# Performance work log

Hardware: AMD Instinct MI355X
Metric: run time of the kernel (lower is better)

Reference implementation:

```python
import jax, jax.numpy as jnp
import numpy as np

B, N, D, H = 4, 2048, 256, 4
DH = D // H          # 64
SCALE = DH ** (-0.5)
LN_EPS = 1e-5


def setup_inputs() -> dict:
    key = jax.random.key(0)
    ks = jax.random.split(key, 16)
    g = lambda k, shape, fan_in: jax.random.normal(k, shape, jnp.float32) / np.sqrt(fan_in)
    # Weights stored as [in, out] (pre-transposed vs torch Linear)
    return {
        "x0": jax.random.normal(ks[0], (B, N, D), jnp.float32),
        "x1": jax.random.normal(ks[1], (B, N, D), jnp.float32),
        "Wqk": g(ks[2], (D, D), D), "bqk": jnp.zeros((D,), jnp.float32),
        "Wv": g(ks[3], (D, D), D), "bv": jnp.zeros((D,), jnp.float32),
        "Wout": g(ks[4], (D, D), D), "bout": jnp.zeros((D,), jnp.float32),
        "Wf1": g(ks[5], (2 * D, 2 * D), 2 * D), "bf1": jnp.zeros((2 * D,), jnp.float32),
        "ln_g": jnp.ones((2 * D,), jnp.float32), "ln_b": jnp.zeros((2 * D,), jnp.float32),
        "Wf2": g(ks[6], (2 * D, D), 2 * D), "bf2": jnp.zeros((D,), jnp.float32),
    }


def _split_heads(t):
    # [B,N,D] -> [B,H,N,DH]
    b, n, _ = t.shape
    return t.reshape(b, n, H, DH).transpose(0, 2, 1, 3)


def _merge_heads(t):
    # [B,H,N,DH] -> [B,N,D]
    b, h, n, dh = t.shape
    return t.transpose(0, 2, 1, 3).reshape(b, n, h * dh)


def _layernorm(x, g, b):
    mu = jnp.mean(x, axis=-1, keepdims=True)
    var = jnp.mean(jnp.square(x - mu), axis=-1, keepdims=True)
    return (x - mu) * jax.lax.rsqrt(var + LN_EPS) * g + b


def reference(x0, x1, Wqk, bqk, Wv, bv, Wout, bout, Wf1, bf1, ln_g, ln_b, Wf2, bf2):
    qk0 = _split_heads(x0 @ Wqk + bqk)   # [B,H,N,DH]
    qk1 = _split_heads(x1 @ Wqk + bqk)
    v0 = _split_heads(x0 @ Wv + bv)
    v1 = _split_heads(x1 @ Wv + bv)

    ss = SCALE ** 0.5
    sim = jnp.einsum('bhid,bhjd->bhij', qk0 * ss, qk1 * ss)  # shared score matrix
    attn01 = jax.nn.softmax(sim, axis=-1)   # normalize over j
    attn10 = jax.nn.softmax(sim, axis=-2)   # normalize over i (== softmax(sim^T) transposed)
    m0 = jnp.einsum('bhij,bhjd->bhid', attn01, v1)
    m1 = jnp.einsum('bhji,bhjd->bhid', attn10, v0)

    m0 = _merge_heads(m0) @ Wout + bout   # [B,N,D]
    m1 = _merge_heads(m1) @ Wout + bout

    def ffn(x):
        h = x @ Wf1 + bf1                 # [B,N,2D]
        h = jax.nn.gelu(_layernorm(h, ln_g, ln_b), approximate=False)
        return h @ Wf2 + bf2              # [B,N,D]

    y0 = x0 + ffn(jnp.concatenate([x0, m0], axis=-1))
    y1 = x1 + ffn(jnp.concatenate([x1, m1], axis=-1))
    return (y0, y1)
```

## Files before the change

kernel.cpp:

```cpp
#include <hip/hip_runtime.h>
#include <hip/hip_bf16.h>
#include <math.h>

typedef __bf16 bf16;
typedef __attribute__((ext_vector_type(8))) __bf16 bf16x8;
typedef __attribute__((ext_vector_type(4))) __bf16 bf16x4;
typedef __attribute__((ext_vector_type(2))) __bf16 bf16x2;
typedef __attribute__((ext_vector_type(4))) float f32x4;
typedef __attribute__((ext_vector_type(16))) float f32x16;
typedef __attribute__((ext_vector_type(4))) unsigned u32x4;

#define MFMA(a,b,c)   __builtin_amdgcn_mfma_f32_16x16x32_bf16(a,b,c,0,0,0)
#define MFMA32(a,b,c) __builtin_amdgcn_mfma_f32_32x32x16_bf16(a,b,c,0,0,0)

static constexpr int Bb = 4, Nn = 2048, Hh = 4;
static constexpr float SS2 = 0.4246609001440095f;

__device__ __forceinline__ void lds16(const bf16* src, bf16* dst) {
  __builtin_amdgcn_global_load_lds(
      (const __attribute__((address_space(1))) void*)src,
      (__attribute__((address_space(3))) void*)dst, 16, 0, 0);
}

__device__ __forceinline__ f32x16 zero16() {
  f32x16 t;
#pragma unroll
  for (int i = 0; i < 16; ++i) t[i] = 0.f;
  return t;
}

__global__ __launch_bounds__(256) void prep_k(
    const float* Wqk, const float* Wv, const float* Wout, const float* bout,
    const float* Wf1, const float* Wf2, const float* x0, const float* x1,
    bf16* wqkv_t, bf16* wout_b, bf16* wfold_t, bf16* wf1b_t, bf16* wf2_t,
    bf16* xb0, bf16* xb1) {
  const int bid = blockIdx.x, tid = threadIdx.x;
  if (bid < 128) {
    __shared__ float LT[64][65];
    const float* src; bf16* dst;
    int srcLD, dstLD, r0, c0, rbase;
    int t = bid;
    if (t < 16) {
      src = Wqk; srcLD = 256; r0 = (t >> 2) * 64; c0 = (t & 3) * 64;
      dst = wqkv_t; dstLD = 256; rbase = 0;
    } else if (t < 32) { t -= 16;
      src = Wv; srcLD = 256; r0 = (t >> 2) * 64; c0 = (t & 3) * 64;
      dst = wqkv_t + 256 * 256; dstLD = 256; rbase = 0;
    } else if (t < 64) { t -= 32;
      src = Wf1; srcLD = 512; r0 = (t >> 3) * 64; c0 = (t & 7) * 64;
      dst = wfold_t; dstLD = 512; rbase = 0;
    } else if (t < 96) { t -= 64;
      src = Wf1; srcLD = 512; r0 = 256 + (t >> 3) * 64; c0 = (t & 7) * 64;
      dst = wf1b_t; dstLD = 256; rbase = 256;
    } else { t -= 96;
      src = Wf2; srcLD = 256; r0 = (t >> 2) * 64; c0 = (t & 3) * 64;
      dst = wf2_t; dstLD = 512; rbase = 0;
    }
#pragma unroll
    for (int i = 0; i < 4; ++i) {
      int rr = (tid >> 4) + i * 16;
      int cc = (tid & 15) * 4;
      f32x4 v = *reinterpret_cast<const f32x4*>(&src[(size_t)(r0 + rr) * srcLD + c0 + cc]);
      LT[rr][cc] = v[0]; LT[rr][cc + 1] = v[1]; LT[rr][cc + 2] = v[2]; LT[rr][cc + 3] = v[3];
    }
    __syncthreads();
    int n = tid >> 2, kc = (tid & 3) * 16;
    bf16x8 o0, o1;
#pragma unroll
    for (int i = 0; i < 8; ++i) o0[i] = (bf16)LT[kc + i][n];
#pragma unroll
    for (int i = 0; i < 8; ++i) o1[i] = (bf16)LT[kc + 8 + i][n];
    bf16* dp = dst + (size_t)(c0 + n) * dstLD + (r0 - rbase) + kc;
    *reinterpret_cast<bf16x8*>(dp) = o0;
    *reinterpret_cast<bf16x8*>(dp + 8) = o1;
    return;
  }
  int id = bid - 128;
  if (id < 96) {
    int base = id * 1024 + tid * 4;
#pragma unroll
    for (int i = 0; i < 4; ++i) {
      int e = base + i;
      if (e < 65536) wout_b[e] = (bf16)Wout[e];
      else { int id3 = e - 65536; int r = id3 >> 8, k = id3 & 255;
             wout_b[e] = (r == 0) ? (bf16)bout[k] : (bf16)0.f; }
    }
    return;
  }
  id -= 96;
  if (id < 4096) {
    int j = id * 256 + tid;
    const float* xs = (j < 524288) ? x0 : x1;
    bf16* xd = (j < 524288) ? xb0 : xb1;
    int jj = (j < 524288) ? j : j - 524288;
    f32x4 v = *reinterpret_cast<const f32x4*>(&xs[(size_t)jj * 4]);
    bf16x4 o; o[0] = (bf16)v[0]; o[1] = (bf16)v[1]; o[2] = (bf16)v[2]; o[3] = (bf16)v[3];
    *reinterpret_cast<bf16x4*>(&xd[(size_t)jj * 4]) = o;
  }
}

__global__ __launch_bounds__(256, 2) void qkvfold_k(
    const bf16* xb0, const bf16* xb1, const bf16* wqkv_t,
    const float* bqk, const float* bv,
    bf16* qks0, bf16* qks1, bf16* vT0, bf16* vT1,
    const bf16* wout_b, const bf16* wf1b_t, const float* bf1,
    bf16* wfold_t, float* bfold) {
  const int fid = blockIdx.x;
  const bool fold = fid >= 512;
  int bx, by, bz;
  if (!fold) {
    bx = ((fid & 7) << 3) + ((fid >> 3) & 7);
    by = (fid >> 6) & 3;
    bz = fid >> 8;
  } else {
    int id = fid - 512;
    bx = id % 3; by = id / 3; bz = 0;
  }

  const bf16* Aa = fold ? wout_b : (bz ? xb1 : xb0);
  const bf16* Wt = fold ? wf1b_t : wqkv_t;

  const int tid = threadIdx.x;
  const int lane = tid & 63;
  const int w = tid >> 6;
  const int wr = w >> 1, wc = w & 1;
  const int m0r = bx * 128;
  const int n0 = by * 128;
  const int r15 = lane & 15, g = lane >> 4, rb = r15 & 7;
  const int l3 = lane >> 3, l7 = lane & 7;
  const int swzc = (l7 ^ l3) * 8;

  __shared__ bf16 At[2][8192];
  __shared__ bf16 Bt[2][8192];

  const bf16* aA = Aa + (size_t)(m0r + w*32 + l3) * 256 + swzc;
  const bf16* bB = Wt + (size_t)(n0 + w*32 + l3) * 256 + swzc;
  const int adst = (w*32) * 64;

  auto stage = [&](int buf, int kc) {
#pragma unroll
    for (int i = 0; i < 4; i++)
      lds16(aA + kc*64 + (size_t)i * 8 * 256, &At[buf][adst + i*512]);
#pragma unroll
    for (int i = 0; i < 4; i++)
      lds16(bB + kc*64 + (size_t)i * 8 * 256, &Bt[buf][adst + i*512]);
  };

  f32x4 acc[4][4];
#pragma unroll
  for (int i = 0; i < 4; i++)
#pragma unroll
    for (int j = 0; j < 4; j++) acc[i][j] = f32x4{0.f, 0.f, 0.f, 0.f};

  const int rx0 = ((0*4 + g) ^ rb) << 4;
  const int rx1 = ((1*4 + g) ^ rb) << 4;

  auto compute = [&](int cur) {
    const char* Ap = (const char*)&At[cur][0];
    const char* Bp = (const char*)&Bt[cur][0];
    __builtin_amdgcn_s_setprio(1);
#pragma unroll
    for (int ks = 0; ks < 2; ++ks) {
      const int rx = ks ? rx1 : rx0;
      bf16x8 af[4], bfr[4];
#pragma unroll
      for (int mf = 0; mf < 4; ++mf)
        af[mf] = *reinterpret_cast<const bf16x8*>(Ap + (wr*64 + mf*16 + r15) * 128 + rx);
#pragma unroll
      for (int nf = 0; nf < 4; ++nf)
        bfr[nf] = *reinterpret_cast<const bf16x8*>(Bp + (wc*64 + nf*16 + r15) * 128 + rx);
#pragma unroll
      for (int mf = 0; mf < 4; ++mf)
#pragma unroll
        for (int nf = 0; nf < 4; ++nf)
          acc[mf][nf] = MFMA(af[mf], bfr[nf], acc[mf][nf]);
    }
    __builtin_amdgcn_s_setprio(0);
  };

  stage(0, 0);
  int cur = 0;
  for (int kc = 0; kc < 3; ++kc) {
    stage(cur ^ 1, kc + 1);
    asm volatile("s_waitcnt vmcnt(8)" ::: "memory");
    __builtin_amdgcn_sched_barrier(0);
    __builtin_amdgcn_s_barrier();
    __builtin_amdgcn_sched_barrier(0);
    compute(cur);
    asm volatile("s_waitcnt lgkmcnt(0)" ::: "memory");
    __builtin_amdgcn_sched_barrier(0);
    __builtin_amdgcn_s_barrier();
    __builtin_amdgcn_sched_barrier(0);
    cur ^= 1;
  }
  asm volatile("s_waitcnt vmcnt(0)" ::: "memory");
  __builtin_amdgcn_sched_barrier(0);
  __builtin_amdgcn_s_barrier();
  __builtin_amdgcn_sched_barrier(0);
  compute(cur);

  if (!fold) {
    bf16* qks = bz ? qks1 : qks0;
    bf16* vT  = bz ? vT1  : vT0;
    if (by < 2) {
#pragma unroll
      for (int mf = 0; mf < 4; ++mf)
#pragma unroll
        for (int nf = 0; nf < 4; ++nf) {
          f32x4 c = acc[mf][nf];
          int cg = n0 + wc*64 + nf*16 + r15;
#pragma unroll
          for (int r = 0; r < 4; ++r) {
            int rg = m0r + wr*64 + mf*16 + g*4 + r;
            int b = rg >> 11, n = rg & 2047;
            float val = (c[r] + bqk[cg]) * SS2;
            int h = cg >> 6, dh = cg & 63;
            qks[(((size_t)(b*Hh + h)) * Nn + n) * 64 + dh] = (bf16)val;
          }
        }
    } else {
      __syncthreads();
      char* T = (char*)&At[0][0];
#pragma unroll
      for (int mf = 0; mf < 4; ++mf)
#pragma unroll
        for (int nf = 0; nf < 4; ++nf) {
          f32x4 c = acc[mf][nf];
          int cl = wc*64 + nf*16 + r15;
          float bvv = bv[(by - 2) * 128 + cl];
          int rl = wr*64 + mf*16 + g*4;
          bf16x4 o;
          o[0] = (bf16)(c[0] + bvv); o[1] = (bf16)(c[1] + bvv);
          o[2] = (bf16)(c[2] + bvv); o[3] = (bf16)(c[3] + bvv);
          int boff = cl*256 + ((rl*2) ^ ((cl & 15) << 4));
          *reinterpret_cast<bf16x4*>(T + boff) = o;
        }
      __syncthreads();
      const int cl = tid >> 1, nh = tid & 1;
      const int c2 = (by - 2) * 128 + cl;
      const int h = c2 >> 6, dh = c2 & 63;
      const int b = m0r >> 11, nbase = (m0r & 2047) + nh*64;
      bf16* dst = vT + (((size_t)(b*Hh + h)) * 64 + dh) * 2048 + nbase;
#pragma unroll
      for (int i = 0; i < 8; ++i) {
        int nl = nh*64 + i*8;
        int boff = cl*256 + ((nl*2) ^ ((cl & 15) << 4));
        *reinterpret_cast<uint4*>(dst + i*8) = *reinterpret_cast<const uint4*>(T + boff);
      }
    }
  } else {
#pragma unroll
    for (int mf = 0; mf < 4; ++mf)
#pragma unroll
      for (int nf = 0; nf < 4; ++nf) {
        f32x4 c = acc[mf][nf];
        int cg = n0 + wc*64 + nf*16 + r15;
#pragma unroll
        for (int r = 0; r < 4; ++r) {
          int rg = m0r + wr*64 + mf*16 + g*4 + r;
          if (rg < 256) wfold_t[(size_t)cg * 512 + 256 + rg] = (bf16)c[r];
          else if (rg == 256) bfold[cg] = c[r] + bf1[cg];
        }
      }
  }
}

template<int MODE, int BN, int MINW, int REMAP>
__global__ __launch_bounds__(256, MINW) void gemm_k(
    const bf16* Aa0, const bf16* Aa1, const bf16* Ac0, const bf16* Ac1,
    const bf16* Wt, const float* bias,
    bf16* ob0, bf16* ob1, float* of0, float* of1) {
  constexpr int KD  = 512;
  constexpr int LDA = (MODE == 4) ? 512 : 256;
  constexpr int NKC = KD / 64;
  constexpr int NF  = BN / 32;

  int bx = blockIdx.x, by = blockIdx.y, bz = blockIdx.z;
  if constexpr (REMAP == 1) {
    int id = blockIdx.x + 64 * (blockIdx.y + 4 * blockIdx.z);
    bx = ((id & 7) << 3) + ((id >> 3) & 7);
    by = (id >> 6) & 3;
    bz = id >> 8;
  }

  const bf16* Aa = bz ? Aa1 : Aa0;
  const bf16* Ac = bz ? Ac1 : Ac0;
  bf16*  ob = bz ? ob1 : ob0;
  float* of = bz ? of1 : of0;

  const int tid = threadIdx.x;
  const int lane = tid & 63;
  const int w = tid >> 6;
  const int wr = w >> 1, wc = w & 1;
  const int m0r = bx * 128;
  const int n0 = by * BN;
  const int r15 = lane & 15, g = lane >> 4, rb = r15 & 7;
  const int l3 = lane >> 3, l7 = lane & 7;
  const int swzc = (l7 ^ l3) * 8;

  __shared__ bf16 At[2][8192];
  __shared__ bf16 Bt[2][BN * 64];

  const bf16* aA = Aa + (size_t)(m0r + w*32 + l3) * LDA + swzc;
  const bf16* aC = (MODE == 3) ? (Ac + (size_t)(m0r + w*32 + l3) * 256 + swzc) : nullptr;
  const bf16* bB = Wt + (size_t)(n0 + w*(BN/4) + l3) * KD + swzc;
  const int adst = (w*32) * 64;
  const int bdst = (w*(BN/4)) * 64;

  auto stage = [&](int buf, int kc) {
    const bf16* ab; int kcol;
    if constexpr (MODE == 3) {
      if (kc < 4) { ab = aA; kcol = kc * 64; } else { ab = aC; kcol = (kc - 4) * 64; }
    } else { ab = aA; kcol = kc * 64; }
#pragma unroll
    for (int i = 0; i < 4; i++)
      lds16(ab + kcol + (size_t)i * 8 * LDA, &At[buf][adst + i*512]);
#pragma unroll
    for (int i = 0; i < NF; i++)
      lds16(bB + kc*64 + (size_t)i * 8 * KD, &Bt[buf][bdst + i*512]);
  };

  f32x4 acc[4][NF];
#pragma unroll
  for (int i = 0; i < 4; i++)
#pragma unroll
    for (int j = 0; j < NF; j++) acc[i][j] = f32x4{0.f, 0.f, 0.f, 0.f};

  const int rx0 = ((0*4 + g) ^ rb) << 4;
  const int rx1 = ((1*4 + g) ^ rb) << 4;

  auto compute = [&](int cur) {
    const char* Ap = (const char*)&At[cur][0];
    const char* Bp = (const char*)&Bt[cur][0];
    __builtin_amdgcn_s_setprio(1);
#pragma unroll
    for (int ks = 0; ks < 2; ++ks) {
      const int rx = ks ? rx1 : rx0;
      bf16x8 af[4], bfr[NF];
#pragma unroll
      for (int mf = 0; mf < 4; ++mf)
        af[mf] = *reinterpret_cast<const bf16x8*>(Ap + (wr*64 + mf*16 + r15) * 128 + rx);
#pragma unroll
      for (int nf = 0; nf < NF; ++nf)
        bfr[nf] = *reinterpret_cast<const bf16x8*>(Bp + (wc*(BN/2) + nf*16 + r15) * 128 + rx);
#pragma unroll
      for (int mf = 0; mf < 4; ++mf)
#pragma unroll
        for (int nf = 0; nf < NF; ++nf)
          acc[mf][nf] = MFMA(af[mf], bfr[nf], acc[mf][nf]);
    }
    __builtin_amdgcn_s_setprio(0);
  };

  stage(0, 0);
  int cur = 0;
  for (int kc = 0; kc < NKC - 1; ++kc) {
    stage(cur ^ 1, kc + 1);
    if constexpr (NF == 4) asm volatile("s_waitcnt vmcnt(8)" ::: "memory");
    else                   asm volatile("s_waitcnt vmcnt(6)" ::: "memory");
    __builtin_amdgcn_sched_barrier(0);
    __builtin_amdgcn_s_barrier();
    __builtin_amdgcn_sched_barrier(0);
    compute(cur);
    asm volatile("s_waitcnt lgkmcnt(0)" ::: "memory");
    __builtin_amdgcn_sched_barrier(0);
    __builtin_amdgcn_s_barrier();
    __builtin_amdgcn_sched_barrier(0);
    cur ^= 1;
  }
  asm volatile("s_waitcnt vmcnt(0)" ::: "memory");
  __builtin_amdgcn_sched_barrier(0);
  __builtin_amdgcn_s_barrier();
  __builtin_amdgcn_sched_barrier(0);
  compute(cur);

#pragma unroll
  for (int mf = 0; mf < 4; ++mf)
#pragma unroll
    for (int nf = 0; nf < NF; ++nf) {
      f32x4 c = acc[mf][nf];
      int cg = n0 + wc*(BN/2) + nf*16 + r15;
#pragma unroll
      for (int r = 0; r < 4; ++r) {
        int rg = m0r + wr*64 + mf*16 + g*4 + r;
        if constexpr (MODE == 3) {
          ob[(size_t)rg * 512 + cg] = (bf16)(c[r] + bias[cg]);
        } else {
          of[(size_t)rg * 256 + cg] = c[r] + bias[cg] + (float)Ac[(size_t)rg * 256 + cg];
        }
      }
    }
}

__global__ __launch_bounds__(512, 4) void attn_k(
    const bf16* qks0, const bf16* qks1, const bf16* vT0, const bf16* vT1,
    bf16* m0o, bf16* m1o) {
  const int B = blockIdx.x + 16 * (blockIdx.y + 16 * blockIdx.z);
  const int xcd = B & 7, kk = B >> 3;
  const int group = 4 * xcd + (kk >> 4);
  const int it = kk & 15;
  const int bh = group & 15, dir = group >> 4;

  const bf16* Q  = (dir ? qks1 : qks0) + (size_t)bh * (Nn * 64);
  const bf16* Kp = (dir ? qks0 : qks1) + (size_t)bh * (Nn * 64);
  const bf16* Vp = (dir ? vT0  : vT1 ) + (size_t)bh * (64 * Nn);
  bf16* out = dir ? m1o : m0o;
  const int b = bh >> 2, h = bh & 3;

  const int tid = threadIdx.x, lane = tid & 63, w = tid >> 6;
  const int ig = w >> 1, hj = w & 1;
  const int l31 = lane & 31, hi = lane >> 5, xr = l31 & 7;
  const int iw = it * 128 + ig * 32;

  __shared__ char smem[65536];
  bf16* KV = (bf16*)smem;
  const int kbase = hj * 8192;
  const int vbase = 16384 + hj * 8192;

  bf16x8 qf[4];
#pragma unroll
  for (int kt = 0; kt < 4; ++kt)
    qf[kt] = *reinterpret_cast<const bf16x8*>(
        &Q[(size_t)(iw + l31) * 64 + kt*16 + hi*8]);

  f32x16 acc[2]; acc[0] = zero16(); acc[1] = zero16();
  float rsum = 0.f;

  const int l3 = lane >> 3, l7 = lane & 7;
  const int swz = ((l7 ^ l3) * 8);
  const bf16* ks0 = Kp + (size_t)(ig*16 +     l3) * 64 + swz;
  const bf16* ks1 = Kp + (size_t)(ig*16 + 8 + l3) * 64 + swz;
  const bf16* vs0 = Vp + (size_t)(ig*16 +     l3) * 2048 + swz;
  const bf16* vs1 = Vp + (size_t)(ig*16 + 8 + l3) * 2048 + swz;
  const int kd0 = (ig*16    ) * 64;
  const int kd1 = (ig*16 + 8) * 64;

  auto stage = [&](int buf, int j0) {
    lds16(ks0 + (size_t)j0 * 64, KV + kbase + buf*4096 + kd0);
    lds16(ks1 + (size_t)j0 * 64, KV + kbase + buf*4096 + kd1);
    lds16(vs0 + j0,              KV + vbase + buf*4096 + kd0);
    lds16(vs1 + j0,              KV + vbase + buf*4096 + kd1);
  };

  int kby[2][4], vby[2][4];
#pragma unroll
  for (int jm = 0; jm < 2; ++jm)
#pragma unroll
    for (int kt = 0; kt < 4; ++kt)
      kby[jm][kt] = (jm*32 + l31) * 128 + (((2*kt + hi) ^ xr) << 4);
#pragma unroll
  for (int nt = 0; nt < 2; ++nt)
#pragma unroll
    for (int gg = 0; gg < 4; ++gg)
      vby[nt][gg] = (nt*32 + l31) * 128 + (((2*gg + hi) ^ xr) << 4);

  auto compute_tile = [&](int cur) {
    const char* Kb = (const char*)(KV + kbase + cur*4096);
    const char* Vb = (const char*)(KV + vbase + cur*4096);
    f32x16 st[2];
    __builtin_amdgcn_s_setprio(1);
#pragma unroll
    for (int jm = 0; jm < 2; ++jm) {
      f32x16 t = zero16();
#pragma unroll
      for (int kt = 0; kt < 4; ++kt) {
        bf16x8 kf = *reinterpret_cast<const bf16x8*>(Kb + kby[jm][kt]);
        t = MFMA32(kf, qf[kt], t);
      }
      st[jm] = t;
    }
    __builtin_amdgcn_s_setprio(0);
    bf16x8 pa[4];
#pragma unroll
    for (int jm = 0; jm < 2; ++jm) {
      unsigned dw[8];
#pragma unroll
      for (int s = 0; s < 8; ++s) {
        float e0 = __builtin_amdgcn_exp2f(st[jm][2*s]);
        float e1 = __builtin_amdgcn_exp2f(st[jm][2*s + 1]);
        rsum += e0 + e1;
        asm("v_cvt_pk_bf16_f32 %0, %1, %2" : "=v"(dw[s]) : "v"(e0), "v"(e1));
      }
#pragma unroll
      for (int kt2 = 0; kt2 < 2; ++kt2) {
        unsigned a0 = dw[4*kt2 + 0], b0 = dw[4*kt2 + 2];
        unsigned a1 = dw[4*kt2 + 1], b1 = dw[4*kt2 + 3];
        asm volatile("v_permlane32_swap_b32 %0, %1" : "+v"(a0), "+v"(b0));
        asm volatile("v_permlane32_swap_b32 %0, %1" : "+v"(a1), "+v"(b1));
        u32x4 uu; uu[0] = a0; uu[1] = a1; uu[2] = b0; uu[3] = b1;
        pa[jm*2 + kt2] = __builtin_bit_cast(bf16x8, uu);
      }
    }
    __builtin_amdgcn_s_setprio(1);
#pragma unroll
    for (int gg = 0; gg < 4; ++gg) {
#pragma unroll
      for (int nt = 0; nt < 2; ++nt) {
        bf16x8 vf = *reinterpret_cast<const bf16x8*>(Vb + vby[nt][gg]);
        acc[nt] = MFMA32(pa[gg], vf, acc[nt]);
      }
    }
    __builtin_amdgcn_s_setprio(0);
  };

  const int jt0 = hj << 4;
  stage(0, jt0 << 6);
  int cur = 0;
  for (int t = 0; t < 15; ++t) {
    stage(cur ^ 1, (jt0 + t + 1) << 6);
    asm volatile("s_waitcnt vmcnt(4)" ::: "memory");
    __builtin_amdgcn_s_barrier();
    compute_tile(cur);
    asm volatile("s_waitcnt lgkmcnt(0)" ::: "memory");
    __builtin_amdgcn_s_barrier();
    cur ^= 1;
  }
  asm volatile("s_waitcnt vmcnt(0)" ::: "memory");
  __builtin_amdgcn_s_barrier();
  compute_tile(cur);

  rsum += __shfl_xor(rsum, 32);
  __syncthreads();
  float* Ex = (float*)smem;
  if (hj == 1) {
#pragma unroll
    for (int nt = 0; nt < 2; ++nt)
#pragma unroll
      for (int r = 0; r < 16; ++r)
        Ex[(ig*33 + nt*16 + r) * 64 + lane] = acc[nt][r];
    Ex[(ig*33 + 32) * 64 + lane] = rsum;
  }
  __syncthreads();
  if (hj == 0) {
    float tot = rsum + Ex[(ig*33 + 32) * 64 + lane];
    float* Rt2 = (float*)(smem + 49152);
    if (lane < 32) Rt2[ig*32 + l31] = tot;
    f32x4 rv[4];
#pragma unroll
    for (int q = 0; q < 4; ++q)
      rv[q] = *reinterpret_cast<const f32x4*>(&Rt2[ig*32 + 8*q + 4*hi]);
#pragma unroll
    for (int r = 0; r < 16; ++r) {
      float inv = 1.0f / rv[r >> 2][r & 3];
      int row = iw + (r & 3) + 8*(r >> 2) + 4*hi;
#pragma unroll
      for (int nt = 0; nt < 2; ++nt) {
        float o = acc[nt][r] + Ex[(ig*33 + nt*16 + r) * 64 + lane];
        int col = h*64 + nt*32 + l31;
        out[((size_t)b * Nn + row) * 256 + col] = (bf16)(o * inv);
      }
    }
  }
}

__global__ __launch_bounds__(256) void ln_gelu_k(
    bf16* hg, const float* g, const float* bb) {
  const int row = (blockIdx.x << 2) + (threadIdx.x >> 6);
  const int lane = threadIdx.x & 63;
  bf16* hr = hg + (size_t)row * 512 + lane * 8;
  bf16x8 v = *reinterpret_cast<const bf16x8*>(hr);
  float f[8];
  float s = 0.f, sq = 0.f;
#pragma unroll
  for (int i = 0; i < 8; ++i) { f[i] = (float)v[i]; s += f[i]; sq += f[i]*f[i]; }
#pragma unroll
  for (int m = 1; m < 64; m <<= 1) { s += __shfl_xor(s, m); sq += __shfl_xor(sq, m); }
  float mu = s * (1.f / 512.f);
  float var = sq * (1.f / 512.f) - mu * mu;
  float rsv = rsqrtf(var + 1e-5f);
  f32x4 g0 = *reinterpret_cast<const f32x4*>(&g[lane*8]);
  f32x4 g1 = *reinterpret_cast<const f32x4*>(&g[lane*8 + 4]);
  f32x4 b0 = *reinterpret_cast<const f32x4*>(&bb[lane*8]);
  f32x4 b1 = *reinterpret_cast<const f32x4*>(&bb[lane*8 + 4]);
  bf16x8 o;
#pragma unroll
  for (int i = 0; i < 8; ++i) {
    float gv = (i < 4) ? g0[i] : g1[i-4];
    float bv = (i < 4) ? b0[i] : b1[i-4];
    float xn = (f[i] - mu) * rsv * gv + bv;
    float ge = 0.5f * xn * (1.f + erff(xn * 0.70710678118f));
    o[i] = (bf16)ge;
  }
  *reinterpret_cast<bf16x8*>(hr) = o;
}

extern "C" void kernel_launch(void* const* d_in, const int* in_sizes, int n_in,
                              void* d_out, int out_size, void* d_ws, size_t ws_size,
                              hipStream_t stream) {
  (void)in_sizes; (void)n_in; (void)out_size; (void)ws_size;
  const float* x0   = (const float*)d_in[0];
  const float* x1   = (const float*)d_in[1];
  const float* Wqk  = (const float*)d_in[2];
  const float* bqk  = (const float*)d_in[3];
  const float* Wv   = (const float*)d_in[4];
  const float* bv   = (const float*)d_in[5];
  const float* Wout = (const float*)d_in[6];
  const float* bout = (const float*)d_in[7];
  const float* Wf1  = (const float*)d_in[8];
  const float* bf1  = (const float*)d_in[9];
  const float* ln_g = (const float*)d_in[10];
  const float* ln_b = (const float*)d_in[11];
  const float* Wf2  = (const float*)d_in[12];
  const float* bf2  = (const float*)d_in[13];
  float* y = (float*)d_out;

  bf16* p = (bf16*)d_ws;
  bf16* wqkv_t = p; p += 131072;
  bf16* wout_b = p; p += 98304;
  bf16* wfold_t = p; p += 262144;
  bf16* wf1b_t = p; p += 131072;
  bf16* wf2_t  = p; p += 131072;
  float* bfold = (float*)p; p += 1024;
  bf16* xb0  = p; p += 2097152;
  bf16* xb1  = p; p += 2097152;
  bf16* qks0 = p; p += 2097152;
  bf16* qks1 = p; p += 2097152;
  bf16* vT0  = p; p += 2097152;
  bf16* vT1  = p; p += 2097152;
  bf16* m0   = p; p += 2097152;
  bf16* m1   = p; p += 2097152;
  bf16* hg0  = p; p += 4194304;
  bf16* hg1  = p; p += 4194304;

  dim3 blk(256);
  prep_k<<<4320, blk, 0, stream>>>(Wqk, Wv, Wout, bout, Wf1, Wf2, x0, x1,
                                   wqkv_t, wout_b, wfold_t, wf1b_t, wf2_t, xb0, xb1);
  qkvfold_k<<<dim3(524), blk, 0, stream>>>(
      xb0, xb1, wqkv_t, bqk, bv, qks0, qks1, vT0, vT1,
      wout_b, wf1b_t, bf1, wfold_t, bfold);
  attn_k<<<dim3(16, 16, 2), dim3(512), 0, stream>>>(qks0, qks1, vT0, vT1, m0, m1);
  gemm_k<3,128,2,1><<<dim3(64, 4, 2), blk, 0, stream>>>(
      xb0, xb1, m0, m1, wfold_t, bfold,
      hg0, hg1, nullptr, nullptr);
  ln_gelu_k<<<dim3(4096), blk, 0, stream>>>(hg0, ln_g, ln_b);
  gemm_k<4,64,3,0><<<dim3(64, 4, 2), blk, 0, stream>>>(
      hg0, hg1, xb0, xb1, wf2_t, bf2,
      nullptr, nullptr, y, y + 2097152);
}
```

Before: 110.6 us.

## Fuse x fp32->bf16 conversion into QKV GEMM and attention tail blocks

The QKV projection now reads x0/x1 directly as fp32 through registers and converts to bf16 while writing into LDS, instead of relying on a separate conversion pass in prep_k. The bf16 copies of x still needed by the later FFN GEMMs are produced by 512 extra blocks appended to the attention launch, so prep_k shrinks to weight preparation only. The GEMM pipeline is restructured so the global loads for the next tile are issued before compute and the LDS writes happen after it. This trades a separate memory pass for doubled fp32 A-tile read traffic and register-staged loads in the GEMM, and it adds tail work to the attention grid.

```diff
diff --git a/kernel.cpp b/kernel.cpp
--- a/kernel.cpp
+++ b/kernel.cpp
@@ -31,9 +31,8 @@
 
 __global__ __launch_bounds__(256) void prep_k(
     const float* Wqk, const float* Wv, const float* Wout, const float* bout,
-    const float* Wf1, const float* Wf2, const float* x0, const float* x1,
-    bf16* wqkv_t, bf16* wout_b, bf16* wfold_t, bf16* wf1b_t, bf16* wf2_t,
-    bf16* xb0, bf16* xb1) {
+    const float* Wf1, const float* Wf2,
+    bf16* wqkv_t, bf16* wout_b, bf16* wfold_t, bf16* wf1b_t, bf16* wf2_t) {
   const int bid = blockIdx.x, tid = threadIdx.x;
   if (bid < 128) {
     __shared__ float LT[64][65];
@@ -85,22 +84,11 @@
       else { int id3 = e - 65536; int r = id3 >> 8, k = id3 & 255;
              wout_b[e] = (r == 0) ? (bf16)bout[k] : (bf16)0.f; }
     }
-    return;
-  }
-  id -= 96;
-  if (id < 4096) {
-    int j = id * 256 + tid;
-    const float* xs = (j < 524288) ? x0 : x1;
-    bf16* xd = (j < 524288) ? xb0 : xb1;
-    int jj = (j < 524288) ? j : j - 524288;
-    f32x4 v = *reinterpret_cast<const f32x4*>(&xs[(size_t)jj * 4]);
-    bf16x4 o; o[0] = (bf16)v[0]; o[1] = (bf16)v[1]; o[2] = (bf16)v[2]; o[3] = (bf16)v[3];
-    *reinterpret_cast<bf16x4*>(&xd[(size_t)jj * 4]) = o;
   }
 }
 
 __global__ __launch_bounds__(256, 2) void qkvfold_k(
-    const bf16* xb0, const bf16* xb1, const bf16* wqkv_t,
+    const float* x0, const float* x1, const bf16* wqkv_t,
     const float* bqk, const float* bv,
     bf16* qks0, bf16* qks1, bf16* vT0, bf16* vT1,
     const bf16* wout_b, const bf16* wf1b_t, const float* bf1,
@@ -117,8 +105,8 @@
     bx = id % 3; by = id / 3; bz = 0;
   }
 
-  const bf16* Aa = fold ? wout_b : (bz ? xb1 : xb0);
-  const bf16* Wt = fold ? wf1b_t : wqkv_t;
+  const float* Xf = bz ? x1 : x0;
+  const bf16*  Wt = fold ? wf1b_t : wqkv_t;
 
   const int tid = threadIdx.x;
   const int lane = tid & 63;
@@ -133,14 +121,40 @@
   __shared__ bf16 At[2][8192];
   __shared__ bf16 Bt[2][8192];
 
-  const bf16* aA = Aa + (size_t)(m0r + w*32 + l3) * 256 + swzc;
-  const bf16* bB = Wt + (size_t)(n0 + w*32 + l3) * 256 + swzc;
+  const float* aF = Xf + (size_t)(m0r + w*32 + l3) * 256 + swzc;
+  const bf16*  aB = wout_b + (size_t)(m0r + w*32 + l3) * 256 + swzc;
+  const bf16*  bB = Wt + (size_t)(n0 + w*32 + l3) * 256 + swzc;
   const int adst = (w*32) * 64;
 
-  auto stage = [&](int buf, int kc) {
-#pragma unroll
-    for (int i = 0; i < 4; i++)
-      lds16(aA + kc*64 + (size_t)i * 8 * 256, &At[buf][adst + i*512]);
+  f32x4 arf[8];
+  u32x4 arb[4];
+  auto loadA = [&](int kc) {
+    if (!fold) {
+#pragma unroll
+      for (int i = 0; i < 4; i++) {
+        arf[2*i]   = *reinterpret_cast<const f32x4*>(aF + kc*64 + (size_t)i * 8 * 256);
+        arf[2*i+1] = *reinterpret_cast<const f32x4*>(aF + kc*64 + (size_t)i * 8 * 256 + 4);
+      }
+    } else {
+#pragma unroll
+      for (int i = 0; i < 4; i++)
+        arb[i] = *reinterpret_cast<const u32x4*>(aB + kc*64 + (size_t)i * 8 * 256);
+    }
+  };
+  auto writeA = [&](int buf) {
+#pragma unroll
+    for (int i = 0; i < 4; i++) {
+      bf16x8 o;
+      if (!fold) {
+#pragma unroll
+        for (int j = 0; j < 4; j++) { o[j] = (bf16)arf[2*i][j]; o[4+j] = (bf16)arf[2*i+1][j]; }
+      } else {
+        o = __builtin_bit_cast(bf16x8, arb[i]);
+      }
+      *reinterpret_cast<bf16x8*>(&At[buf][adst + i*512 + lane*8]) = o;
+    }
+  };
+  auto stageB = [&](int buf, int kc) {
 #pragma unroll
     for (int i = 0; i < 4; i++)
       lds16(bB + kc*64 + (size_t)i * 8 * 256, &Bt[buf][adst + i*512]);
@@ -178,25 +192,23 @@
     __builtin_amdgcn_s_setprio(0);
   };
 
-  stage(0, 0);
+  loadA(0);
+  stageB(0, 0);
+  asm volatile("s_waitcnt vmcnt(4)" ::: "memory");
+  writeA(0);
+  asm volatile("s_waitcnt vmcnt(0) lgkmcnt(0)" ::: "memory");
+  __builtin_amdgcn_s_barrier();
   int cur = 0;
   for (int kc = 0; kc < 3; ++kc) {
-    stage(cur ^ 1, kc + 1);
-    asm volatile("s_waitcnt vmcnt(8)" ::: "memory");
-    __builtin_amdgcn_sched_barrier(0);
+    loadA(kc + 1);
+    stageB(cur ^ 1, kc + 1);
+    compute(cur);
+    asm volatile("s_waitcnt vmcnt(0)" ::: "memory");
+    writeA(cur ^ 1);
+    asm volatile("s_waitcnt lgkmcnt(0)" ::: "memory");
     __builtin_amdgcn_s_barrier();
-    __builtin_amdgcn_sched_barrier(0);
-    compute(cur);
-    asm volatile("s_waitcnt lgkmcnt(0)" ::: "memory");
-    __builtin_amdgcn_sched_barrier(0);
-    __builtin_amdgcn_s_barrier();
-    __builtin_amdgcn_sched_barrier(0);
     cur ^= 1;
   }
-  asm volatile("s_waitcnt vmcnt(0)" ::: "memory");
-  __builtin_amdgcn_sched_barrier(0);
-  __builtin_amdgcn_s_barrier();
-  __builtin_amdgcn_sched_barrier(0);
   compute(cur);
 
   if (!fold) {
@@ -394,8 +406,24 @@
 
 __global__ __launch_bounds__(512, 4) void attn_k(
     const bf16* qks0, const bf16* qks1, const bf16* vT0, const bf16* vT1,
-    bf16* m0o, bf16* m1o) {
-  const int B = blockIdx.x + 16 * (blockIdx.y + 16 * blockIdx.z);
+    bf16* m0o, bf16* m1o,
+    const float* x0, const float* x1, bf16* xb0, bf16* xb1) {
+  const int B = blockIdx.x;
+  if (B >= 512) {
+    const int id = B - 512;
+    const float* xs = (id < 256) ? x0 : x1;
+    bf16* xd = (id < 256) ? xb0 : xb1;
+    const int cid = id & 255;
+    const int tid = threadIdx.x;
+#pragma unroll
+    for (int i = 0; i < 4; ++i) {
+      size_t v4 = (size_t)cid * 2048 + i * 512 + tid;
+      f32x4 v = *reinterpret_cast<const f32x4*>(&xs[v4 * 4]);
+      bf16x4 o; o[0] = (bf16)v[0]; o[1] = (bf16)v[1]; o[2] = (bf16)v[2]; o[3] = (bf16)v[3];
+      *reinterpret_cast<bf16x4*>(&xd[v4 * 4]) = o;
+    }
+    return;
+  }
   const int xcd = B & 7, kk = B >> 3;
   const int group = 4 * xcd + (kk >> 4);
   const int it = kk & 15;
@@ -623,12 +651,13 @@
   bf16* hg1  = p; p += 4194304;
 
   dim3 blk(256);
-  prep_k<<<4320, blk, 0, stream>>>(Wqk, Wv, Wout, bout, Wf1, Wf2, x0, x1,
-                                   wqkv_t, wout_b, wfold_t, wf1b_t, wf2_t, xb0, xb1);
+  prep_k<<<224, blk, 0, stream>>>(Wqk, Wv, Wout, bout, Wf1, Wf2,
+                                  wqkv_t, wout_b, wfold_t, wf1b_t, wf2_t);
   qkvfold_k<<<dim3(524), blk, 0, stream>>>(
-      xb0, xb1, wqkv_t, bqk, bv, qks0, qks1, vT0, vT1,
+      x0, x1, wqkv_t, bqk, bv, qks0, qks1, vT0, vT1,
       wout_b, wf1b_t, bf1, wfold_t, bfold);
-  attn_k<<<dim3(16, 16, 2), dim3(512), 0, stream>>>(qks0, qks1, vT0, vT1, m0, m1);
+  attn_k<<<dim3(1024), dim3(512), 0, stream>>>(qks0, qks1, vT0, vT1, m0, m1,
+                                               x0, x1, xb0, xb1);
   gemm_k<3,128,2,1><<<dim3(64, 4, 2), blk, 0, stream>>>(
       xb0, xb1, m0, m1, wfold_t, bfold,
       hg0, hg1, nullptr, nullptr);
```

New measurement: 112.2 us. Within noise of the previous version (+1.4%).
